# Kernel optimization log

Hardware: AMD Instinct MI355X
Metric: run time of the kernel (lower is better)

Reference implementation:

```python
import jax, jax.numpy as jnp
import numpy as np

D = 128   # d_model
K = 128   # knn neighbors
NL = 4    # point transformer layers
EPS = 1e-5


def _timestep_embedding(t, dim):
    half = dim // 2
    freqs = jnp.exp(-jnp.log(10000.0) * jnp.arange(half, dtype=jnp.float32) / (half - 1))
    args = t.astype(jnp.float32)[:, None] * freqs[None, :]          # [B, half]
    return jnp.concatenate([jnp.sin(args), jnp.cos(args)], axis=-1)  # [B, dim]


def _layernorm(x, g, b):
    m = jnp.mean(x, axis=-1, keepdims=True)
    v = jnp.mean((x - m) ** 2, axis=-1, keepdims=True)
    return (x - m) / jnp.sqrt(v + EPS) * g + b


def _pt_layer(xyz, feat, Wq, bq, Wk, bk, Wv, bv, Wp1, bp1, Wp2, bp2, gamma, Wpr, bpr):
    # full pairwise squared distance [B,N,N]
    sq = jnp.sum(xyz * xyz, axis=-1)
    dist = sq[:, :, None] + sq[:, None, :] - 2.0 * jnp.einsum('bnd,bmd->bnm', xyz, xyz)
    _, idx = jax.lax.top_k(-dist, K)                 # k smallest -> [B,N,K]
    gather = jax.vmap(lambda p, i: p[i])             # per-batch gather along N
    nxyz = gather(xyz, idx)                          # [B,N,K,3]
    nfeat = gather(feat, idx)                        # [B,N,K,D]
    q = (feat @ Wq + bq)[:, :, None, :]              # [B,N,1,D]
    k = nfeat @ Wk + bk                              # [B,N,K,D]
    v = nfeat @ Wv + bv                              # [B,N,K,D]
    rel = xyz[:, :, None, :] - nxyz                  # [B,N,K,3]
    pe = jax.nn.relu(rel @ Wp1 + bp1) @ Wp2 + bp2    # [B,N,K,D]
    attn = jax.nn.softmax(jnp.sum(q - k + pe, axis=-1, keepdims=True), axis=-2)  # over K
    agg = jnp.sum(attn * (v + pe), axis=2)           # [B,N,D]
    return feat + gamma * (agg @ Wpr + bpr)


def reference(xyz, feat, x_t, t,
              pt_Wq, pt_bq, pt_Wk, pt_bk, pt_Wv, pt_bv,
              pt_Wp1, pt_bp1, pt_Wp2, pt_bp2, pt_gamma, pt_Wproj, pt_bproj,
              tW1, tb1, tW2, tb2,
              nW1, nb1, ng1, nbeta1, nW2, nb2, ng2, nbeta2, nW3, nb3):
    fused = feat
    for i in range(NL):
        fused = _pt_layer(xyz, fused,
                          pt_Wq[i], pt_bq[i], pt_Wk[i], pt_bk[i], pt_Wv[i], pt_bv[i],
                          pt_Wp1[i], pt_bp1[i], pt_Wp2[i], pt_bp2[i],
                          pt_gamma[i], pt_Wproj[i], pt_bproj[i])
    # DDPM head
    temb = _timestep_embedding(t, D)                 # [B,D]
    temb = jax.nn.relu(temb @ tW1 + tb1) @ tW2 + tb2
    temb = jnp.broadcast_to(temb[:, None, :], fused.shape[:2] + (D,))
    h = jnp.concatenate([x_t, fused, temb], axis=-1)  # [B,N,3+2D]
    h = jax.nn.relu(_layernorm(h @ nW1 + nb1, ng1, nbeta1))
    h = jax.nn.relu(_layernorm(h @ nW2 + nb2, ng2, nbeta2))
    return h @ nW3 + nb3                              # [B,N,3]


def setup_inputs() -> dict:
    key = jax.random.key(0)
    ks = jax.random.split(key, 32)
    B, N = 2, 2048
    rn = lambda k, shape, s=0.02: (jax.random.normal(k, shape) * s).astype(jnp.float32)
    in_dim = 3 + D + D
    return {
        'xyz': jax.random.normal(ks[0], (B, N, 3), dtype=jnp.float32),
        'feat': jax.random.normal(ks[1], (B, N, D), dtype=jnp.float32),
        'x_t': jax.random.normal(ks[2], (B, N, 3), dtype=jnp.float32),
        't': jax.random.randint(ks[3], (B,), 0, 1000),
        'pt_Wq': rn(ks[4], (NL, D, D)), 'pt_bq': jnp.zeros((NL, D), jnp.float32),
        'pt_Wk': rn(ks[5], (NL, D, D)), 'pt_bk': jnp.zeros((NL, D), jnp.float32),
        'pt_Wv': rn(ks[6], (NL, D, D)), 'pt_bv': jnp.zeros((NL, D), jnp.float32),
        'pt_Wp1': rn(ks[7], (NL, 3, D)), 'pt_bp1': jnp.zeros((NL, D), jnp.float32),
        'pt_Wp2': rn(ks[8], (NL, D, D)), 'pt_bp2': jnp.zeros((NL, D), jnp.float32),
        'pt_gamma': rn(ks[9], (NL,), 0.1),
        'pt_Wproj': rn(ks[10], (NL, D, D)), 'pt_bproj': jnp.zeros((NL, D), jnp.float32),
        'tW1': rn(ks[11], (D, D)), 'tb1': jnp.zeros((D,), jnp.float32),
        'tW2': rn(ks[12], (D, D)), 'tb2': jnp.zeros((D,), jnp.float32),
        'nW1': rn(ks[13], (in_dim, D)), 'nb1': jnp.zeros((D,), jnp.float32),
        'ng1': jnp.ones((D,), jnp.float32), 'nbeta1': jnp.zeros((D,), jnp.float32),
        'nW2': rn(ks[14], (D, D)), 'nb2': jnp.zeros((D,), jnp.float32),
        'ng2': jnp.ones((D,), jnp.float32), 'nbeta2': jnp.zeros((D,), jnp.float32),
        'nW3': rn(ks[15], (D, 3)), 'nb3': jnp.zeros((3,), jnp.float32),
    }
```

## Files before the change

### kernel.cpp

```cpp
#include <hip/hip_runtime.h>
#include <math.h>

#define B_SZ 2
#define N_PTS 2048
#define DM 128
#define KNN 128
#define NLAYER 4
#define ROWS (B_SZ * N_PTS)
#define RBV 4
#define RB8 8
#define EPSLN 1e-5f

__device__ __forceinline__ float waveSum(float v) {
#pragma unroll
  for (int o = 32; o > 0; o >>= 1) v += __shfl_xor(v, o, 64);
  return v;
}
__device__ __forceinline__ float waveMax(float v) {
#pragma unroll
  for (int o = 32; o > 0; o >>= 1) v = fmaxf(v, __shfl_xor(v, o, 64));
  return v;
}
__device__ __forceinline__ float blockSum128(float v, float* s2, int t) {
  float w = waveSum(v);
  __syncthreads();
  if ((t & 63) == 0) s2[t >> 6] = w;
  __syncthreads();
  return s2[0] + s2[1];
}
__device__ __forceinline__ unsigned waveScanIncl(unsigned v, int lane) {
#pragma unroll
  for (int o = 1; o < 64; o <<= 1) {
    unsigned u = (unsigned)__shfl_up((int)v, o, 64);
    if (lane >= o) v += u;
  }
  return v;
}

template <int STRIDE>
__device__ __forceinline__ void gemv8(const float* src, const float* W, int j0,
                                      int cnt, int d, float* a) {
  for (int jj = 0; jj < cnt; jj += 4) {
    int j = j0 + jj;
    float w0 = W[(j + 0) * DM + d], w1 = W[(j + 1) * DM + d];
    float w2 = W[(j + 2) * DM + d], w3 = W[(j + 3) * DM + d];
#pragma unroll
    for (int rr = 0; rr < 8; ++rr) {
      float4 f = *(const float4*)(src + rr * STRIDE + j);
      a[rr] = fmaf(f.x, w0, fmaf(f.y, w1, fmaf(f.z, w2, fmaf(f.w, w3, a[rr]))));
    }
  }
}

__global__ __launch_bounds__(256) void knn_kernel(const float* __restrict__ xyz,
                                                  int* __restrict__ idx) {
  int row = blockIdx.x;
  int b = row >> 11, i = row & (N_PTS - 1);
  const float* xb = xyz + (size_t)b * N_PTS * 3;
  int tid = threadIdx.x;
  int lane = tid & 63, wid = tid >> 6;

  __shared__ unsigned hist[256];
  __shared__ unsigned wred[4];
  __shared__ unsigned sel[2];

  float xi = xb[i * 3 + 0], yi = xb[i * 3 + 1], zi = xb[i * 3 + 2];
  float sqi = xi * xi + yi * yi + zi * zi;

  float p[24];
  {
    const float4* xb4 = (const float4*)xb;
#pragma unroll
    for (int q = 0; q < 6; ++q) {
      float4 v = xb4[tid * 6 + q];
      p[q * 4 + 0] = v.x; p[q * 4 + 1] = v.y; p[q * 4 + 2] = v.z; p[q * 4 + 3] = v.w;
    }
  }
  unsigned key[8];
#pragma unroll
  for (int s = 0; s < 8; ++s) {
    float xj = p[s * 3 + 0], yj = p[s * 3 + 1], zj = p[s * 3 + 2];
    float d = sqi + xj * xj + yj * yj + zj * zj -
              2.0f * (xi * xj + yi * yj + zi * zj);
    unsigned u = __float_as_uint(d);
    key[s] = (u & 0x80000000u) ? ~u : (u | 0x80000000u);
  }

  unsigned prefix = 0;
  unsigned need = KNN;
  for (int shift = 24; shift >= 0; shift -= 8) {
    hist[tid] = 0;
    __syncthreads();
    if (shift == 24) {
#pragma unroll
      for (int s = 0; s < 8; ++s) {
        unsigned bin = key[s] >> 24;
        unsigned long long act = __ballot(1);
        while (act) {
          int src = __builtin_ctzll(act);
          unsigned bsel = (unsigned)__shfl((int)bin, src, 64);
          unsigned long long grp = __ballot(bin == bsel);
          if (lane == src)
            atomicAdd(&hist[bsel], (unsigned)__builtin_popcountll(grp));
          act &= ~grp;
        }
      }
    } else {
#pragma unroll
      for (int s = 0; s < 8; ++s) {
        unsigned k = key[s];
        if ((k >> (shift + 8)) == prefix)
          atomicAdd(&hist[(k >> shift) & 255u], 1u);
      }
    }
    __syncthreads();
    unsigned h = hist[tid];
    unsigned incl = waveScanIncl(h, lane);
    if (lane == 63) wred[wid] = incl;
    __syncthreads();
    unsigned offs = 0;
    for (int w = 0; w < wid; ++w) offs += wred[w];
    incl += offs;
    unsigned excl = incl - h;
    if (excl < need && need <= incl) { sel[0] = (unsigned)tid; sel[1] = need - excl; }
    __syncthreads();
    prefix = (prefix << 8) | sel[0];
    need = sel[1];
  }
  unsigned T = prefix;
  int need_eq = (int)need;

  unsigned clt = 0, ceq = 0;
#pragma unroll
  for (int s = 0; s < 8; ++s) {
    clt += (key[s] < T);
    ceq += (key[s] == T);
  }
  unsigned packed = clt | (ceq << 16);
  unsigned incl = waveScanIncl(packed, lane);
  if (lane == 63) wred[wid] = incl;
  __syncthreads();
  unsigned offs = 0;
  for (int w = 0; w < wid; ++w) offs += wred[w];
  unsigned totAll = wred[0] + wred[1] + wred[2] + wred[3];
  incl += offs;
  unsigned excl = incl - packed;
  int lt_base = (int)(excl & 0xFFFFu);
  int eq_base = (int)(excl >> 16);
  int total_lt = (int)(totAll & 0xFFFFu);

  int* orow = idx + (size_t)row * KNN;
  int lpos = 0, epos = 0;
#pragma unroll
  for (int s = 0; s < 8; ++s) {
    int j = tid * 8 + s;
    unsigned k = key[s];
    if (k < T) {
      orow[lt_base + lpos] = j; lpos++;
    } else if (k == T) {
      int r = eq_base + epos; epos++;
      if (r < need_eq) orow[total_lt + r] = j;
    }
  }
}

__global__ __launch_bounds__(128) void prep_kernel(
    const float* __restrict__ Wq, const float* __restrict__ bq,
    const float* __restrict__ Wk, const float* __restrict__ bk,
    const float* __restrict__ Wp2, const float* __restrict__ bp2,
    float* __restrict__ rs, float* __restrict__ ssum,
    const int* __restrict__ t, const float* __restrict__ tW1,
    const float* __restrict__ tb1, const float* __restrict__ tW2,
    const float* __restrict__ tb2, float* __restrict__ temb) {
  int blk = blockIdx.x, d = threadIdx.x;
  __shared__ float s2[2];
  __shared__ float emb[DM];
  __shared__ float h1[DM];
  if (blk < NLAYER) {
    int l = blk;
    const float* wq = Wq + (size_t)l * DM * DM;
    const float* wk = Wk + (size_t)l * DM * DM;
    const float* wp2 = Wp2 + (size_t)l * DM * DM;
    float a = 0.f, b = 0.f, c = 0.f;
    for (int j = 0; j < DM; ++j) {
      a += wq[d * DM + j];
      b += wk[d * DM + j];
      c += wp2[d * DM + j];
    }
    rs[l * 3 * DM + d] = a;
    rs[l * 3 * DM + DM + d] = b;
    rs[l * 3 * DM + 2 * DM + d] = c;
    float sq = blockSum128(bq[l * DM + d], s2, d);
    float sk = blockSum128(bk[l * DM + d], s2, d);
    float sp = blockSum128(bp2[l * DM + d], s2, d);
    if (d == 0) { ssum[l * 4 + 0] = sq; ssum[l * 4 + 1] = sk; ssum[l * 4 + 2] = sp; }
  } else {
    int b = blk - NLAYER;
    float tv = (float)t[b];
    float lg = logf(10000.0f);
    if (d < 64) {
      float f = expf(-lg * (float)d / 63.0f);
      emb[d] = sinf(tv * f);
    } else {
      float f = expf(-lg * (float)(d - 64) / 63.0f);
      emb[d] = cosf(tv * f);
    }
    __syncthreads();
    float acc = tb1[d];
    for (int j = 0; j < DM; ++j) acc = fmaf(emb[j], tW1[j * DM + d], acc);
    h1[d] = fmaxf(acc, 0.f);
    __syncthreads();
    float acc2 = tb2[d];
    for (int j = 0; j < DM; ++j) acc2 = fmaf(h1[j], tW2[j * DM + d], acc2);
    temb[b * DM + d] = acc2;
  }
}

__global__ __launch_bounds__(256) void vqk_kernel(
    const float* __restrict__ feat, const float* __restrict__ Wv,
    const float* __restrict__ bv, const float* __restrict__ rs,
    const float* __restrict__ ssum, float* __restrict__ Vf,
    float* __restrict__ qsum, float* __restrict__ ksum) {
  int n0 = blockIdx.x * RBV;
  int t = threadIdx.x;
  int d = t & 127, half = t >> 7;
  __shared__ float fr[RBV][DM];
  __shared__ float part[RBV][DM];
  __shared__ float sA[2][RBV];
  __shared__ float sB[2][RBV];
#pragma unroll
  for (int u = 0; u < 2; ++u) {
    int r = half * 2 + u;
    fr[r][d] = feat[(size_t)(n0 + r) * DM + d];
  }
  __syncthreads();
  float acc[RBV] = {0.f, 0.f, 0.f, 0.f};
  int j0 = half * 64;
  for (int jj = 0; jj < 64; jj += 4) {
    int j = j0 + jj;
    float w0 = Wv[(j + 0) * DM + d], w1 = Wv[(j + 1) * DM + d];
    float w2 = Wv[(j + 2) * DM + d], w3 = Wv[(j + 3) * DM + d];
#pragma unroll
    for (int r = 0; r < RBV; ++r) {
      float4 f = *(const float4*)&fr[r][j];
      acc[r] = fmaf(f.x, w0, fmaf(f.y, w1, fmaf(f.z, w2, fmaf(f.w, w3, acc[r]))));
    }
  }
  if (half == 1) {
#pragma unroll
    for (int r = 0; r < RBV; ++r) part[r][d] = acc[r];
  }
  __syncthreads();
  if (half == 0) {
    float bvd = bv[d];
#pragma unroll
    for (int r = 0; r < RBV; ++r)
      Vf[(size_t)(n0 + r) * DM + d] = acc[r] + part[r][d] + bvd;
    int lane = t & 63, wid = (t >> 6) & 1;
    float rsq = rs[d], rsk = rs[DM + d];
#pragma unroll
    for (int r = 0; r < RBV; ++r) {
      float f = fr[r][d];
      float a = waveSum(f * rsq);
      float k = waveSum(f * rsk);
      if (lane == 0) { sA[wid][r] = a; sB[wid][r] = k; }
    }
  }
  __syncthreads();
  if (t < RBV) qsum[n0 + t] = sA[0][t] + sA[1][t] + ssum[0];
  if (t >= 64 && t < 64 + RBV) {
    int r = t - 64;
    ksum[n0 + r] = sB[0][r] + sB[1][r] + ssum[1];
  }
}

template <int LAST>
__global__ __launch_bounds__(512, 2) void fused_layer_kernel(
    const float* __restrict__ xyz, const int* __restrict__ idx,
    const float* __restrict__ fin, const float* __restrict__ Vf_in,
    const float* __restrict__ qsum_in, const float* __restrict__ ksum_in,
    const float* __restrict__ Wp1, const float* __restrict__ bp1,
    const float* __restrict__ rsL, const float* __restrict__ ssL,
    const float* __restrict__ Wp2, const float* __restrict__ bp2,
    const float* __restrict__ Wproj, const float* __restrict__ bproj,
    const float* __restrict__ gamma, int l, float* __restrict__ fout,
    const float* __restrict__ Wv_n, const float* __restrict__ bv_n,
    const float* __restrict__ rs_n, const float* __restrict__ ss_n,
    float* __restrict__ Vf_out, float* __restrict__ qsum_out,
    float* __restrict__ ksum_out,
    const float* __restrict__ x_t, const float* __restrict__ temb,
    const float* __restrict__ nW1, const float* __restrict__ nb1,
    const float* __restrict__ ng1, const float* __restrict__ nbe1,
    const float* __restrict__ nW2, const float* __restrict__ nb2,
    const float* __restrict__ ng2, const float* __restrict__ nbe2,
    const float* __restrict__ nW3, const float* __restrict__ nb3,
    float* __restrict__ out) {
  int n0 = blockIdx.x * RB8;
  int t = threadIdx.x;
  int w = t >> 6, lane = t & 63;
  int q = t >> 7, d = t & 127;
  int b = n0 >> 11;

  __shared__ float4 rel4[RB8][KNN];
  __shared__ int joff[RB8][KNN];
  __shared__ float hrow[RB8][DM];
  __shared__ float zz[RB8][DM];
  float* part = (float*)rel4;

  const float* xb = xyz + (size_t)b * N_PTS * 3;

  {
    int row = n0 + w;
    int i = row & (N_PTS - 1);
    float xi = xb[i * 3 + 0], yi = xb[i * 3 + 1], zi = xb[i * 3 + 2];
    int j1 = idx[(size_t)row * KNN + lane];
    int j2 = idx[(size_t)row * KNN + lane + 64];
    float rx1 = xi - xb[j1 * 3 + 0], ry1 = yi - xb[j1 * 3 + 1], rz1 = zi - xb[j1 * 3 + 2];
    float rx2 = xi - xb[j2 * 3 + 0], ry2 = yi - xb[j2 * 3 + 1], rz2 = zi - xb[j2 * 3 + 2];

    const float4* W1x = (const float4*)Wp1;
    const float4* W1y = (const float4*)(Wp1 + DM);
    const float4* W1z = (const float4*)(Wp1 + 2 * DM);
    const float4* Bp = (const float4*)bp1;
    const float4* W2 = (const float4*)(rsL + 2 * DM);
    float acc1 = 0.f, acc2 = 0.f;
#pragma unroll 8
    for (int qq = 0; qq < DM / 4; ++qq) {
      float4 ax = W1x[qq], ay = W1y[qq], az = W1z[qq], ab = Bp[qq], c = W2[qq];
      float hA = fmaxf(fmaf(rx1, ax.x, fmaf(ry1, ay.x, fmaf(rz1, az.x, ab.x))), 0.f);
      float hB = fmaxf(fmaf(rx1, ax.y, fmaf(ry1, ay.y, fmaf(rz1, az.y, ab.y))), 0.f);
      float hC = fmaxf(fmaf(rx1, ax.z, fmaf(ry1, ay.z, fmaf(rz1, az.z, ab.z))), 0.f);
      float hD = fmaxf(fmaf(rx1, ax.w, fmaf(ry1, ay.w, fmaf(rz1, az.w, ab.w))), 0.f);
      acc1 = fmaf(hA, c.x, fmaf(hB, c.y, fmaf(hC, c.z, fmaf(hD, c.w, acc1))));
      float hE = fmaxf(fmaf(rx2, ax.x, fmaf(ry2, ay.x, fmaf(rz2, az.x, ab.x))), 0.f);
      float hF = fmaxf(fmaf(rx2, ax.y, fmaf(ry2, ay.y, fmaf(rz2, az.y, ab.y))), 0.f);
      float hG = fmaxf(fmaf(rx2, ax.z, fmaf(ry2, ay.z, fmaf(rz2, az.z, ab.z))), 0.f);
      float hH = fmaxf(fmaf(rx2, ax.w, fmaf(ry2, ay.w, fmaf(rz2, az.w, ab.w))), 0.f);
      acc2 = fmaf(hE, c.x, fmaf(hF, c.y, fmaf(hG, c.z, fmaf(hH, c.w, acc2))));
    }
    float qs = qsum_in[row] + ssL[2];
    float l1 = qs - ksum_in[b * N_PTS + j1] + acc1;
    float l2 = qs - ksum_in[b * N_PTS + j2] + acc2;
    float m = waveMax(fmaxf(l1, l2));
    float e1 = __expf(l1 - m), e2 = __expf(l2 - m);
    float s = waveSum(e1 + e2);
    float inv = 1.0f / s;
    rel4[w][lane] = make_float4(rx1, ry1, rz1, e1 * inv);
    rel4[w][lane + 64] = make_float4(rx2, ry2, rz2, e2 * inv);
    joff[w][lane] = j1 * (DM * 4);
    joff[w][lane + 64] = j2 * (DM * 4);
  }
  __syncthreads();

  {
    int d1 = lane, d2 = lane + 64;
    float wx1 = Wp1[d1], wy1 = Wp1[DM + d1], wz1 = Wp1[2 * DM + d1], wb1 = bp1[d1];
    float wx2 = Wp1[d2], wy2 = Wp1[DM + d2], wz2 = Wp1[2 * DM + d2], wb2 = bp1[d2];
    const char* vbase = (const char*)(Vf_in + (size_t)b * N_PTS * DM);
    const char* v1 = vbase + (size_t)d1 * 4;
    const char* v2 = vbase + (size_t)d2 * 4;
    float ha1a = 0.f, ha1b = 0.f, ha2a = 0.f, ha2b = 0.f;
    float va1a = 0.f, va1b = 0.f, va2a = 0.f, va2b = 0.f;
#pragma unroll 4
    for (int k = 0; k < KNN; k += 2) {
      float4 ra = rel4[w][k];
      float4 rb = rel4[w][k + 1];
      int ja = joff[w][k], jb = joff[w][k + 1];
      float Va1 = *(const float*)(v1 + ja);
      float Vb1 = *(const float*)(v1 + jb);
      float Va2 = *(const float*)(v2 + ja);
      float Vb2 = *(const float*)(v2 + jb);
      float hA1 = fmaxf(fmaf(ra.x, wx1, fmaf(ra.y, wy1, fmaf(ra.z, wz1, wb1))), 0.f);
      float hB1 = fmaxf(fmaf(rb.x, wx1, fmaf(rb.y, wy1, fmaf(rb.z, wz1, wb1))), 0.f);
      float hA2 = fmaxf(fmaf(ra.x, wx2, fmaf(ra.y, wy2, fmaf(ra.z, wz2, wb2))), 0.f);
      float hB2 = fmaxf(fmaf(rb.x, wx2, fmaf(rb.y, wy2, fmaf(rb.z, wz2, wb2))), 0.f);
      ha1a = fmaf(ra.w, hA1, ha1a);
      ha1b = fmaf(rb.w, hB1, ha1b);
      ha2a = fmaf(ra.w, hA2, ha2a);
      ha2b = fmaf(rb.w, hB2, ha2b);
      va1a = fmaf(ra.w, Va1, va1a);
      va1b = fmaf(rb.w, Vb1, va1b);
      va2a = fmaf(ra.w, Va2, va2a);
      va2b = fmaf(rb.w, Vb2, va2b);
    }
    hrow[w][d1] = ha1a + ha1b;
    hrow[w][d2] = ha2a + ha2b;
    zz[w][d1] = va1a + va1b;
    zz[w][d2] = va2a + va2b;
  }
  __syncthreads();

  {
    float a[RB8] = {0.f, 0.f, 0.f, 0.f, 0.f, 0.f, 0.f, 0.f};
    gemv8<DM>(&hrow[0][0], Wp2, q * 32, 32, d, a);
    float* pq = part + (q * RB8) * DM + d;
#pragma unroll
    for (int rr = 0; rr < RB8; ++rr) pq[rr * DM] = a[rr];
  }
  __syncthreads();
  {
    int r0 = q * 2, r1 = q * 2 + 1;
    float bpd = bp2[d];
    zz[r0][d] += part[(0 * RB8 + r0) * DM + d] + part[(1 * RB8 + r0) * DM + d] +
                 part[(2 * RB8 + r0) * DM + d] + part[(3 * RB8 + r0) * DM + d] + bpd;
    zz[r1][d] += part[(0 * RB8 + r1) * DM + d] + part[(1 * RB8 + r1) * DM + d] +
                 part[(2 * RB8 + r1) * DM + d] + part[(3 * RB8 + r1) * DM + d] + bpd;
  }
  __syncthreads();

  {
    float a[RB8] = {0.f, 0.f, 0.f, 0.f, 0.f, 0.f, 0.f, 0.f};
    gemv8<DM>(&zz[0][0], Wproj, q * 32, 32, d, a);
    float* pq = part + (q * RB8) * DM + d;
#pragma unroll
    for (int rr = 0; rr < RB8; ++rr) pq[rr * DM] = a[rr];
  }
  __syncthreads();
  {
    int r0 = q * 2, r1 = q * 2 + 1;
    float g = gamma[l];
    float bpr = bproj[d];
    float s0 = part[(0 * RB8 + r0) * DM + d] + part[(1 * RB8 + r0) * DM + d] +
               part[(2 * RB8 + r0) * DM + d] + part[(3 * RB8 + r0) * DM + d] + bpr;
    float s1 = part[(0 * RB8 + r1) * DM + d] + part[(1 * RB8 + r1) * DM + d] +
               part[(2 * RB8 + r1) * DM + d] + part[(3 * RB8 + r1) * DM + d] + bpr;
    float fo0 = fin[(size_t)(n0 + r0) * DM + d] + g * s0;
    float fo1 = fin[(size_t)(n0 + r1) * DM + d] + g * s1;
    if (!LAST) {
      fout[(size_t)(n0 + r0) * DM + d] = fo0;
      fout[(size_t)(n0 + r1) * DM + d] = fo1;
    }
    hrow[r0][d] = fo0;
    hrow[r1][d] = fo1;
  }
  __syncthreads();

  if constexpr (!LAST) {
    {
      int d1 = lane, d2 = lane + 64;
      float fo1 = hrow[w][d1], fo2 = hrow[w][d2];
      float qp = waveSum(fo1 * rs_n[d1] + fo2 * rs_n[d2]);
      float kp = waveSum(fo1 * rs_n[DM + d1] + fo2 * rs_n[DM + d2]);
      if (lane == 0) {
        qsum_out[n0 + w] = qp + ss_n[0];
        ksum_out[n0 + w] = kp + ss_n[1];
      }
    }
    {
      float a[RB8] = {0.f, 0.f, 0.f, 0.f, 0.f, 0.f, 0.f, 0.f};
      gemv8<DM>(&hrow[0][0], Wv_n, q * 32, 32, d, a);
      float* pq = part + (q * RB8) * DM + d;
#pragma unroll
      for (int rr = 0; rr < RB8; ++rr) pq[rr * DM] = a[rr];
    }
    __syncthreads();
    {
      int r0 = q * 2, r1 = q * 2 + 1;
      float bvd = bv_n[d];
      Vf_out[(size_t)(n0 + r0) * DM + d] =
          part[(0 * RB8 + r0) * DM + d] + part[(1 * RB8 + r0) * DM + d] +
          part[(2 * RB8 + r0) * DM + d] + part[(3 * RB8 + r0) * DM + d] + bvd;
      Vf_out[(size_t)(n0 + r1) * DM + d] =
          part[(0 * RB8 + r1) * DM + d] + part[(1 * RB8 + r1) * DM + d] +
          part[(2 * RB8 + r1) * DM + d] + part[(3 * RB8 + r1) * DM + d] + bvd;
    }
  } else {
    __shared__ float h0s[RB8][260];
    {
      int r0 = q * 2, r1 = q * 2 + 1;
#pragma unroll
      for (int rr = r0; rr <= r1; ++rr) {
        h0s[rr][3 + d] = hrow[rr][d];
        h0s[rr][131 + d] = temb[b * DM + d];
        if (d < 3) h0s[rr][d] = x_t[(size_t)(n0 + rr) * 3 + d];
        if (d == 0) h0s[rr][259] = 0.f;
      }
    }
    __syncthreads();

    {
      float a[RB8] = {0.f, 0.f, 0.f, 0.f, 0.f, 0.f, 0.f, 0.f};
      gemv8<260>(&h0s[0][0], nW1, q * 64, 64, d, a);
      if (q == 3) {
        for (int j = 256; j < 259; ++j) {
          float wv = nW1[j * DM + d];
#pragma unroll
          for (int rr = 0; rr < RB8; ++rr) a[rr] = fmaf(h0s[rr][j], wv, a[rr]);
        }
      }
      float* pq = part + (q * RB8) * DM + d;
#pragma unroll
      for (int rr = 0; rr < RB8; ++rr) pq[rr * DM] = a[rr];
    }
    __syncthreads();
    {
      int r0 = q * 2, r1 = q * 2 + 1;
      float nb = nb1[d];
      zz[r0][d] = nb + part[(0 * RB8 + r0) * DM + d] + part[(1 * RB8 + r0) * DM + d] +
                  part[(2 * RB8 + r0) * DM + d] + part[(3 * RB8 + r0) * DM + d];
      zz[r1][d] = nb + part[(0 * RB8 + r1) * DM + d] + part[(1 * RB8 + r1) * DM + d] +
                  part[(2 * RB8 + r1) * DM + d] + part[(3 * RB8 + r1) * DM + d];
    }
    __syncthreads();
    {
      int d1 = lane, d2 = lane + 64;
      float x1 = zz[w][d1], x2 = zz[w][d2];
      float s1 = waveSum(x1 + x2);
      float sq = waveSum(x1 * x1 + x2 * x2);
      float m = s1 * (1.0f / 128.0f);
      float var = sq * (1.0f / 128.0f) - m * m;
      float rstd = rsqrtf(var + EPSLN);
      float y1 = fmaxf((x1 - m) * rstd * ng1[d1] + nbe1[d1], 0.f);
      float y2 = fmaxf((x2 - m) * rstd * ng1[d2] + nbe1[d2], 0.f);
      zz[w][d1] = y1;
      zz[w][d2] = y2;
    }
    __syncthreads();
    {
      float a[RB8] = {0.f, 0.f, 0.f, 0.f, 0.f, 0.f, 0.f, 0.f};
      gemv8<DM>(&zz[0][0], nW2, q * 32, 32, d, a);
      float* pq = part + (q * RB8) * DM + d;
#pragma unroll
      for (int rr = 0; rr < RB8; ++rr) pq[rr * DM] = a[rr];
    }
    __syncthreads();
    {
      int r0 = q * 2, r1 = q * 2 + 1;
      float nb = nb2[d];
      hrow[r0][d] = nb + part[(0 * RB8 + r0) * DM + d] + part[(1 * RB8 + r0) * DM + d] +
                    part[(2 * RB8 + r0) * DM + d] + part[(3 * RB8 + r0) * DM + d];
      hrow[r1][d] = nb + part[(0 * RB8 + r1) * DM + d] + part[(1 * RB8 + r1) * DM + d] +
                    part[(2 * RB8 + r1) * DM + d] + part[(3 * RB8 + r1) * DM + d];
    }
    __syncthreads();
    {
      int d1 = lane, d2 = lane + 64;
      float x1 = hrow[w][d1], x2 = hrow[w][d2];
      float s1 = waveSum(x1 + x2);
      float sq = waveSum(x1 * x1 + x2 * x2);
      float m = s1 * (1.0f / 128.0f);
      float var = sq * (1.0f / 128.0f) - m * m;
      float rstd = rsqrtf(var + EPSLN);
      float y1 = fmaxf((x1 - m) * rstd * ng2[d1] + nbe2[d1], 0.f);
      float y2 = fmaxf((x2 - m) * rstd * ng2[d2] + nbe2[d2], 0.f);
      float p0 = waveSum(y1 * nW3[d1 * 3 + 0] + y2 * nW3[d2 * 3 + 0]);
      float p1 = waveSum(y1 * nW3[d1 * 3 + 1] + y2 * nW3[d2 * 3 + 1]);
      float p2 = waveSum(y1 * nW3[d1 * 3 + 2] + y2 * nW3[d2 * 3 + 2]);
      if (lane == 0) {
        out[(size_t)(n0 + w) * 3 + 0] = p0 + nb3[0];
        out[(size_t)(n0 + w) * 3 + 1] = p1 + nb3[1];
        out[(size_t)(n0 + w) * 3 + 2] = p2 + nb3[2];
      }
    }
  }
}

extern "C" void kernel_launch(void* const* d_in, const int* in_sizes, int n_in,
                              void* d_out, int out_size, void* d_ws,
                              size_t ws_size, hipStream_t stream) {
  const float* xyz = (const float*)d_in[0];
  const float* feat = (const float*)d_in[1];
  const float* x_t = (const float*)d_in[2];
  const int* t = (const int*)d_in[3];
  const float* Wq = (const float*)d_in[4];
  const float* bq = (const float*)d_in[5];
  const float* Wk = (const float*)d_in[6];
  const float* bk = (const float*)d_in[7];
  const float* Wv = (const float*)d_in[8];
  const float* bv = (const float*)d_in[9];
  const float* Wp1 = (const float*)d_in[10];
  const float* bp1 = (const float*)d_in[11];
  const float* Wp2 = (const float*)d_in[12];
  const float* bp2 = (const float*)d_in[13];
  const float* gamma = (const float*)d_in[14];
  const float* Wproj = (const float*)d_in[15];
  const float* bproj = (const float*)d_in[16];
  const float* tW1 = (const float*)d_in[17];
  const float* tb1 = (const float*)d_in[18];
  const float* tW2 = (const float*)d_in[19];
  const float* tb2 = (const float*)d_in[20];
  const float* nW1 = (const float*)d_in[21];
  const float* nb1 = (const float*)d_in[22];
  const float* ng1 = (const float*)d_in[23];
  const float* nbe1 = (const float*)d_in[24];
  const float* nW2 = (const float*)d_in[25];
  const float* nb2 = (const float*)d_in[26];
  const float* ng2 = (const float*)d_in[27];
  const float* nbe2 = (const float*)d_in[28];
  const float* nW3 = (const float*)d_in[29];
  const float* nb3 = (const float*)d_in[30];
  float* out = (float*)d_out;

  char* ws = (char*)d_ws;
  size_t off = 0;
  int* w_idx = (int*)(ws + off); off += (size_t)ROWS * KNN * 4;
  float* w_VfA = (float*)(ws + off); off += (size_t)ROWS * DM * 4;
  float* w_VfB = (float*)(ws + off); off += (size_t)ROWS * DM * 4;
  float* w_qsA = (float*)(ws + off); off += (size_t)ROWS * 4;
  float* w_ksA = (float*)(ws + off); off += (size_t)ROWS * 4;
  float* w_qsB = (float*)(ws + off); off += (size_t)ROWS * 4;
  float* w_ksB = (float*)(ws + off); off += (size_t)ROWS * 4;
  float* w_fA = (float*)(ws + off); off += (size_t)ROWS * DM * 4;
  float* w_fB = (float*)(ws + off); off += (size_t)ROWS * DM * 4;
  float* w_temb = (float*)(ws + off); off += (size_t)B_SZ * DM * 4;
  float* w_rs = (float*)(ws + off); off += (size_t)NLAYER * 3 * DM * 4;
  float* w_ssum = (float*)(ws + off); off += (size_t)NLAYER * 4 * 4;

  knn_kernel<<<ROWS, 256, 0, stream>>>(xyz, w_idx);
  prep_kernel<<<NLAYER + B_SZ, 128, 0, stream>>>(Wq, bq, Wk, bk, Wp2, bp2,
                                                 w_rs, w_ssum, t, tW1, tb1,
                                                 tW2, tb2, w_temb);
  vqk_kernel<<<ROWS / RBV, 256, 0, stream>>>(feat, Wv, bv, w_rs, w_ssum,
                                             w_VfA, w_qsA, w_ksA);

  const float* fins[4] = {feat, w_fA, w_fB, w_fA};
  float* fouts[4] = {w_fA, w_fB, w_fA, w_fB};
  const float* VfIn[4] = {w_VfA, w_VfB, w_VfA, w_VfB};
  float* VfOut[4] = {w_VfB, w_VfA, w_VfB, w_VfA};
  const float* qsIn[4] = {w_qsA, w_qsB, w_qsA, w_qsB};
  float* qsOut[4] = {w_qsB, w_qsA, w_qsB, w_qsA};
  const float* ksIn[4] = {w_ksA, w_ksB, w_ksA, w_ksB};
  float* ksOut[4] = {w_ksB, w_ksA, w_ksB, w_ksA};

  for (int l = 0; l < NLAYER; ++l) {
    const float* rsL = w_rs + (size_t)l * 3 * DM;
    const float* ssL = w_ssum + (size_t)l * 4;
    int ln = (l + 1 < NLAYER) ? (l + 1) : l;
    const float* rsN = w_rs + (size_t)ln * 3 * DM;
    const float* ssN = w_ssum + (size_t)ln * 4;
    if (l < NLAYER - 1) {
      fused_layer_kernel<0><<<ROWS / RB8, 512, 0, stream>>>(
          xyz, w_idx, fins[l], VfIn[l], qsIn[l], ksIn[l],
          Wp1 + (size_t)l * 3 * DM, bp1 + (size_t)l * DM, rsL, ssL,
          Wp2 + (size_t)l * DM * DM, bp2 + (size_t)l * DM,
          Wproj + (size_t)l * DM * DM, bproj + (size_t)l * DM, gamma, l,
          fouts[l], Wv + (size_t)ln * DM * DM, bv + (size_t)ln * DM, rsN, ssN,
          VfOut[l], qsOut[l], ksOut[l], x_t, w_temb, nW1, nb1, ng1, nbe1, nW2,
          nb2, ng2, nbe2, nW3, nb3, out);
    } else {
      fused_layer_kernel<1><<<ROWS / RB8, 512, 0, stream>>>(
          xyz, w_idx, fins[l], VfIn[l], qsIn[l], ksIn[l],
          Wp1 + (size_t)l * 3 * DM, bp1 + (size_t)l * DM, rsL, ssL,
          Wp2 + (size_t)l * DM * DM, bp2 + (size_t)l * DM,
          Wproj + (size_t)l * DM * DM, bproj + (size_t)l * DM, gamma, l,
          fouts[l], Wv + (size_t)ln * DM * DM, bv + (size_t)ln * DM, rsN, ssN,
          VfOut[l], qsOut[l], ksOut[l], x_t, w_temb, nW1, nb1, ng1, nbe1, nW2,
          nb2, ng2, nbe2, nW3, nb3, out);
    }
  }
}
```

Measured before the change: 190.3 us.

## Interleave V feature layout for float2 gathers and drop a block barrier

V rows are now stored in an interleaved order: feature d goes to slot 2*(d&63)+(d>>6). Each lane can then fetch its two features (d and d+64) for a gathered neighbour with one 8-byte load instead of two scattered 4-byte loads. The producers of Vf in both kernels write to the new slot so the layout stays consistent. A __syncthreads between building the per-wave rel4/joff tables and consuming them is also removed, relying on each wave reading only its own slice. That relies on wave-synchronous LDS visibility without an explicit barrier or fence.

```diff
diff --git a/kernel.cpp b/kernel.cpp
--- a/kernel.cpp
+++ b/kernel.cpp
@@ -10,6 +10,8 @@
 #define RBV 4
 #define RB8 8
 #define EPSLN 1e-5f
+
+__device__ __forceinline__ int vfslot(int d) { return 2 * (d & 63) + (d >> 6); }
 
 __device__ __forceinline__ float waveSum(float v) {
 #pragma unroll
@@ -253,9 +255,10 @@
   __syncthreads();
   if (half == 0) {
     float bvd = bv[d];
+    int slot = vfslot(d);
 #pragma unroll
     for (int r = 0; r < RBV; ++r)
-      Vf[(size_t)(n0 + r) * DM + d] = acc[r] + part[r][d] + bvd;
+      Vf[(size_t)(n0 + r) * DM + slot] = acc[r] + part[r][d] + bvd;
     int lane = t & 63, wid = (t >> 6) & 1;
     float rsq = rs[d], rsk = rs[DM + d];
 #pragma unroll
@@ -350,26 +353,21 @@
     joff[w][lane] = j1 * (DM * 4);
     joff[w][lane + 64] = j2 * (DM * 4);
   }
-  __syncthreads();
 
   {
     int d1 = lane, d2 = lane + 64;
     float wx1 = Wp1[d1], wy1 = Wp1[DM + d1], wz1 = Wp1[2 * DM + d1], wb1 = bp1[d1];
     float wx2 = Wp1[d2], wy2 = Wp1[DM + d2], wz2 = Wp1[2 * DM + d2], wb2 = bp1[d2];
-    const char* vbase = (const char*)(Vf_in + (size_t)b * N_PTS * DM);
-    const char* v1 = vbase + (size_t)d1 * 4;
-    const char* v2 = vbase + (size_t)d2 * 4;
+    const char* vbase = (const char*)(Vf_in + (size_t)b * N_PTS * DM) + (size_t)lane * 8;
     float ha1a = 0.f, ha1b = 0.f, ha2a = 0.f, ha2b = 0.f;
     float va1a = 0.f, va1b = 0.f, va2a = 0.f, va2b = 0.f;
 #pragma unroll 4
     for (int k = 0; k < KNN; k += 2) {
       float4 ra = rel4[w][k];
       float4 rb = rel4[w][k + 1];
-      int ja = joff[w][k], jb = joff[w][k + 1];
-      float Va1 = *(const float*)(v1 + ja);
-      float Vb1 = *(const float*)(v1 + jb);
-      float Va2 = *(const float*)(v2 + ja);
-      float Vb2 = *(const float*)(v2 + jb);
+      int2 jj = *(const int2*)&joff[w][k];
+      float2 Va = *(const float2*)(vbase + jj.x);
+      float2 Vb = *(const float2*)(vbase + jj.y);
       float hA1 = fmaxf(fmaf(ra.x, wx1, fmaf(ra.y, wy1, fmaf(ra.z, wz1, wb1))), 0.f);
       float hB1 = fmaxf(fmaf(rb.x, wx1, fmaf(rb.y, wy1, fmaf(rb.z, wz1, wb1))), 0.f);
       float hA2 = fmaxf(fmaf(ra.x, wx2, fmaf(ra.y, wy2, fmaf(ra.z, wz2, wb2))), 0.f);
@@ -378,10 +376,10 @@
       ha1b = fmaf(rb.w, hB1, ha1b);
       ha2a = fmaf(ra.w, hA2, ha2a);
       ha2b = fmaf(rb.w, hB2, ha2b);
-      va1a = fmaf(ra.w, Va1, va1a);
-      va1b = fmaf(rb.w, Vb1, va1b);
-      va2a = fmaf(ra.w, Va2, va2a);
-      va2b = fmaf(rb.w, Vb2, va2b);
+      va1a = fmaf(ra.w, Va.x, va1a);
+      va1b = fmaf(rb.w, Vb.x, va1b);
+      va2a = fmaf(ra.w, Va.y, va2a);
+      va2b = fmaf(rb.w, Vb.y, va2b);
     }
     hrow[w][d1] = ha1a + ha1b;
     hrow[w][d2] = ha2a + ha2b;
@@ -457,10 +455,11 @@
     {
       int r0 = q * 2, r1 = q * 2 + 1;
       float bvd = bv_n[d];
-      Vf_out[(size_t)(n0 + r0) * DM + d] =
+      int slot = vfslot(d);
+      Vf_out[(size_t)(n0 + r0) * DM + slot] =
           part[(0 * RB8 + r0) * DM + d] + part[(1 * RB8 + r0) * DM + d] +
           part[(2 * RB8 + r0) * DM + d] + part[(3 * RB8 + r0) * DM + d] + bvd;
-      Vf_out[(size_t)(n0 + r1) * DM + d] =
+      Vf_out[(size_t)(n0 + r1) * DM + slot] =
           part[(0 * RB8 + r1) * DM + d] + part[(1 * RB8 + r1) * DM + d] +
           part[(2 * RB8 + r1) * DM + d] + part[(3 * RB8 + r1) * DM + d] + bvd;
     }
```

Result: slower. 195.2 us (+2.6%).

## Assign one wavefront per query row in kNN radix select

Applied to the files above, without the earlier changes.

The kNN kernel now gives each query row to a single 64-lane wavefront instead of a whole 256-thread block. Each lane holds 32 candidate keys, and each wave keeps a private histogram in shared memory. Block-wide __syncthreads and the cross-wave scans are replaced by wave-level ballot, shuffle and scan. This removes block barriers and shared-memory reductions, at the cost of more registers per thread and longer serial ballot loops on the first radix pass.

```diff
diff --git a/kernel.cpp b/kernel.cpp
--- a/kernel.cpp
+++ b/kernel.cpp
@@ -54,46 +54,44 @@
 
 __global__ __launch_bounds__(256) void knn_kernel(const float* __restrict__ xyz,
                                                   int* __restrict__ idx) {
-  int row = blockIdx.x;
+  int w = threadIdx.x >> 6, lane = threadIdx.x & 63;
+  int row = blockIdx.x * 4 + w;
   int b = row >> 11, i = row & (N_PTS - 1);
   const float* xb = xyz + (size_t)b * N_PTS * 3;
-  int tid = threadIdx.x;
-  int lane = tid & 63, wid = tid >> 6;
-
-  __shared__ unsigned hist[256];
-  __shared__ unsigned wred[4];
-  __shared__ unsigned sel[2];
+
+  __shared__ unsigned hist[4][256];
 
   float xi = xb[i * 3 + 0], yi = xb[i * 3 + 1], zi = xb[i * 3 + 2];
   float sqi = xi * xi + yi * yi + zi * zi;
 
-  float p[24];
+  unsigned key[32];
   {
-    const float4* xb4 = (const float4*)xb;
-#pragma unroll
-    for (int q = 0; q < 6; ++q) {
-      float4 v = xb4[tid * 6 + q];
-      p[q * 4 + 0] = v.x; p[q * 4 + 1] = v.y; p[q * 4 + 2] = v.z; p[q * 4 + 3] = v.w;
-    }
-  }
-  unsigned key[8];
-#pragma unroll
-  for (int s = 0; s < 8; ++s) {
-    float xj = p[s * 3 + 0], yj = p[s * 3 + 1], zj = p[s * 3 + 2];
-    float d = sqi + xj * xj + yj * yj + zj * zj -
-              2.0f * (xi * xj + yi * yj + zi * zj);
-    unsigned u = __float_as_uint(d);
-    key[s] = (u & 0x80000000u) ? ~u : (u | 0x80000000u);
+    const float4* pb = (const float4*)xb + (size_t)lane * 24;
+#pragma unroll
+    for (int c = 0; c < 8; ++c) {
+      float4 v0 = pb[c * 3 + 0], v1 = pb[c * 3 + 1], v2 = pb[c * 3 + 2];
+      float px[4] = {v0.x, v0.w, v1.z, v2.y};
+      float py[4] = {v0.y, v1.x, v1.w, v2.z};
+      float pz[4] = {v0.z, v1.y, v2.x, v2.w};
+#pragma unroll
+      for (int u = 0; u < 4; ++u) {
+        float d = sqi + px[u] * px[u] + py[u] * py[u] + pz[u] * pz[u] -
+                  2.0f * (xi * px[u] + yi * py[u] + zi * pz[u]);
+        unsigned uu = __float_as_uint(d);
+        key[c * 4 + u] = (uu & 0x80000000u) ? ~uu : (uu | 0x80000000u);
+      }
+    }
   }
 
   unsigned prefix = 0;
   unsigned need = KNN;
   for (int shift = 24; shift >= 0; shift -= 8) {
-    hist[tid] = 0;
-    __syncthreads();
+#pragma unroll
+    for (int qq = 0; qq < 4; ++qq) hist[w][lane * 4 + qq] = 0;
+    __threadfence_block();
     if (shift == 24) {
 #pragma unroll
-      for (int s = 0; s < 8; ++s) {
+      for (int s = 0; s < 32; ++s) {
         unsigned bin = key[s] >> 24;
         unsigned long long act = __ballot(1);
         while (act) {
@@ -101,49 +99,49 @@
           unsigned bsel = (unsigned)__shfl((int)bin, src, 64);
           unsigned long long grp = __ballot(bin == bsel);
           if (lane == src)
-            atomicAdd(&hist[bsel], (unsigned)__builtin_popcountll(grp));
+            atomicAdd(&hist[w][bsel], (unsigned)__builtin_popcountll(grp));
           act &= ~grp;
         }
       }
     } else {
 #pragma unroll
-      for (int s = 0; s < 8; ++s) {
+      for (int s = 0; s < 32; ++s) {
         unsigned k = key[s];
         if ((k >> (shift + 8)) == prefix)
-          atomicAdd(&hist[(k >> shift) & 255u], 1u);
+          atomicAdd(&hist[w][(k >> shift) & 255u], 1u);
       }
     }
-    __syncthreads();
-    unsigned h = hist[tid];
-    unsigned incl = waveScanIncl(h, lane);
-    if (lane == 63) wred[wid] = incl;
-    __syncthreads();
-    unsigned offs = 0;
-    for (int w = 0; w < wid; ++w) offs += wred[w];
-    incl += offs;
-    unsigned excl = incl - h;
-    if (excl < need && need <= incl) { sel[0] = (unsigned)tid; sel[1] = need - excl; }
-    __syncthreads();
-    prefix = (prefix << 8) | sel[0];
-    need = sel[1];
+    __threadfence_block();
+    unsigned h0 = hist[w][lane * 4 + 0], h1 = hist[w][lane * 4 + 1];
+    unsigned h2 = hist[w][lane * 4 + 2], h3 = hist[w][lane * 4 + 3];
+    unsigned sl = h0 + h1 + h2 + h3;
+    unsigned incl = waveScanIncl(sl, lane);
+    unsigned excl = incl - sl;
+    unsigned c0 = excl + h0, c1 = c0 + h1, c2 = c1 + h2, c3 = c2 + h3;
+    unsigned sd = 0xFFFFFFFFu, sr = 0;
+    if (excl < need && need <= c0) { sd = lane * 4 + 0; sr = need - excl; }
+    else if (c0 < need && need <= c1) { sd = lane * 4 + 1; sr = need - c0; }
+    else if (c1 < need && need <= c2) { sd = lane * 4 + 2; sr = need - c1; }
+    else if (c2 < need && need <= c3) { sd = lane * 4 + 3; sr = need - c2; }
+    unsigned long long mk = __ballot(sd != 0xFFFFFFFFu);
+    int src = __builtin_ctzll(mk);
+    sd = (unsigned)__shfl((int)sd, src, 64);
+    sr = (unsigned)__shfl((int)sr, src, 64);
+    prefix = (prefix << 8) | sd;
+    need = sr;
   }
   unsigned T = prefix;
   int need_eq = (int)need;
 
   unsigned clt = 0, ceq = 0;
 #pragma unroll
-  for (int s = 0; s < 8; ++s) {
+  for (int s = 0; s < 32; ++s) {
     clt += (key[s] < T);
     ceq += (key[s] == T);
   }
   unsigned packed = clt | (ceq << 16);
   unsigned incl = waveScanIncl(packed, lane);
-  if (lane == 63) wred[wid] = incl;
-  __syncthreads();
-  unsigned offs = 0;
-  for (int w = 0; w < wid; ++w) offs += wred[w];
-  unsigned totAll = wred[0] + wred[1] + wred[2] + wred[3];
-  incl += offs;
+  unsigned totAll = (unsigned)__shfl((int)incl, 63, 64);
   unsigned excl = incl - packed;
   int lt_base = (int)(excl & 0xFFFFu);
   int eq_base = (int)(excl >> 16);
@@ -152,8 +150,8 @@
   int* orow = idx + (size_t)row * KNN;
   int lpos = 0, epos = 0;
 #pragma unroll
-  for (int s = 0; s < 8; ++s) {
-    int j = tid * 8 + s;
+  for (int s = 0; s < 32; ++s) {
+    int j = lane * 32 + s;
     unsigned k = key[s];
     if (k < T) {
       orow[lt_base + lpos] = j; lpos++;
@@ -606,7 +604,7 @@
   float* w_rs = (float*)(ws + off); off += (size_t)NLAYER * 3 * DM * 4;
   float* w_ssum = (float*)(ws + off); off += (size_t)NLAYER * 4 * 4;
 
-  knn_kernel<<<ROWS, 256, 0, stream>>>(xyz, w_idx);
+  knn_kernel<<<ROWS / 4, 256, 0, stream>>>(xyz, w_idx);
   prep_kernel<<<NLAYER + B_SZ, 128, 0, stream>>>(Wq, bq, Wk, bk, Wp2, bp2,
                                                  w_rs, w_ssum, t, tW1, tb1,
                                                  tW2, tb2, w_temb);
```

Result: slower. 197.9 us (+4.0%).
